# Kernel tuning notes

Hardware: AMD Instinct MI355X
Metric: run time of the kernel (lower is better)

Reference implementation:

```python
import jax, jax.numpy as jnp
import numpy as np

B = 128
N_ATOMS = 4096
NB, NA, NT = 4095, 4094, 4093
MAX_LEN = 5 * NT  # 20465, longest packed column (torsions)
EPS = 1e-8


def setup_inputs() -> dict:
    key = jax.random.key(0)
    ks = jax.random.split(key, 24)
    feats = jnp.zeros((B, MAX_LEN, 9), jnp.float32)
    # col 0: atom type ids
    atoms = jax.random.randint(ks[0], (B, N_ATOMS), 0, 6)
    # col 5: coords, flattened (N_ATOMS, 3)
    coords = jax.random.normal(ks[1], (B, N_ATOMS, 3), jnp.float32) * 5.0
    # col 6: bonds (i, j, type)
    bonds = jnp.stack([
        jax.random.randint(ks[2], (B, NB), 0, N_ATOMS),
        jax.random.randint(ks[3], (B, NB), 0, N_ATOMS),
        jax.random.randint(ks[4], (B, NB), 0, 15)], axis=-1)
    # col 7: angles (i, j, k, type)
    angles = jnp.stack([
        jax.random.randint(ks[5], (B, NA), 0, N_ATOMS),
        jax.random.randint(ks[6], (B, NA), 0, N_ATOMS),
        jax.random.randint(ks[7], (B, NA), 0, N_ATOMS),
        jax.random.randint(ks[8], (B, NA), 0, 13)], axis=-1)
    # col 8: torsions (i, j, k, l, type)
    tors = jnp.stack([
        jax.random.randint(ks[9], (B, NT), 0, N_ATOMS),
        jax.random.randint(ks[10], (B, NT), 0, N_ATOMS),
        jax.random.randint(ks[11], (B, NT), 0, N_ATOMS),
        jax.random.randint(ks[12], (B, NT), 0, N_ATOMS),
        jax.random.randint(ks[13], (B, NT), 0, 25)], axis=-1)
    feats = feats.at[:, :N_ATOMS, 0].set(atoms.astype(jnp.float32))
    feats = feats.at[:, :3 * N_ATOMS, 5].set(coords.reshape(B, -1))
    feats = feats.at[:, :3 * NB, 6].set(bonds.reshape(B, -1).astype(jnp.float32))
    feats = feats.at[:, :4 * NA, 7].set(angles.reshape(B, -1).astype(jnp.float32))
    feats = feats.at[:, :5 * NT, 8].set(tors.reshape(B, -1).astype(jnp.float32))
    lengths = jnp.tile(jnp.array(
        [[N_ATOMS, 0, 0, 0, 0, 3 * N_ATOMS, 3 * NB, 4 * NA, 5 * NT]],
        jnp.int32), (B, 1))
    bond_type = jnp.stack([jnp.ones(15), jax.random.uniform(ks[14], (15,), minval=1.0, maxval=2.0)], -1).astype(jnp.float32)
    angle_type = jnp.stack([jnp.ones(13), jax.random.uniform(ks[15], (13,), minval=1.0, maxval=3.0)], -1).astype(jnp.float32)
    tor_type = jnp.stack([jnp.ones(25), jax.random.uniform(ks[16], (25,), minval=0.0, maxval=3.14)], -1).astype(jnp.float32)
    multiplicity = jax.random.randint(ks[17], (25,), 1, 4)
    opt_pars = jax.random.uniform(ks[18], (47,), minval=0.5, maxval=1.5).astype(jnp.float32)
    return {"features": feats, "lengths": lengths, "bond_type": bond_type,
            "angle_type": angle_type, "tor_type": tor_type,
            "multiplicity": multiplicity, "opt_pars": opt_pars}


def _sample_energy(f, bond_type, angle_type, tor_type, multiplicity, opt_pars):
    coords = f[:3 * N_ATOMS, 5].reshape(-1, 3)                      # [N,3]
    bonds = f[:3 * NB, 6].astype(jnp.int32).reshape(-1, 3)          # [NB,3]
    angles = f[:4 * NA, 7].astype(jnp.int32).reshape(-1, 4)         # [NA,4]
    tors = f[:5 * NT, 8].astype(jnp.int32).reshape(-1, 5)           # [NT,5]

    # bonds: harmonic k*(r - r0)^2
    d = coords[bonds[:, 0]] - coords[bonds[:, 1]]
    r = jnp.sqrt(jnp.sum(d * d, -1) + EPS)
    pb = bond_type[bonds[:, 2]]
    e_bond = opt_pars[0] * jnp.sum(pb[:, 0] * (r - pb[:, 1]) ** 2)

    # angles: harmonic k*(theta - theta0)^2
    v1 = coords[angles[:, 0]] - coords[angles[:, 1]]
    v2 = coords[angles[:, 2]] - coords[angles[:, 1]]
    cosang = jnp.sum(v1 * v2, -1) / (
        jnp.sqrt(jnp.sum(v1 * v1, -1) + EPS) * jnp.sqrt(jnp.sum(v2 * v2, -1) + EPS))
    theta = jnp.arccos(jnp.clip(cosang, -1.0 + 1e-6, 1.0 - 1e-6))
    pa = angle_type[angles[:, 3]]
    e_ang = opt_pars[1] * jnp.sum(pa[:, 0] * (theta - pa[:, 1]) ** 2)

    # torsions: periodic k*(1 + cos(n*phi - delta))
    ci, cj, ck, cl = (coords[tors[:, m]] for m in range(4))
    b1, b2, b3 = cj - ci, ck - cj, cl - ck
    n1 = jnp.cross(b1, b2)
    n2 = jnp.cross(b2, b3)
    b2n = b2 / jnp.sqrt(jnp.sum(b2 * b2, -1, keepdims=True) + EPS)
    m1 = jnp.cross(n1, b2n)
    phi = jnp.arctan2(jnp.sum(m1 * n2, -1), jnp.sum(n1 * n2, -1))
    pt = tor_type[tors[:, 4]]
    n_mult = multiplicity[tors[:, 4]].astype(jnp.float32)
    e_tor = opt_pars[2] * jnp.sum(pt[:, 0] * (1.0 + jnp.cos(n_mult * phi - pt[:, 1])))

    return jnp.stack([e_bond, e_ang, e_tor])


def reference(features, lengths, bond_type, angle_type, tor_type, multiplicity, opt_pars):
    # lengths are uniform across batch (constants above); vmap over batch dim
    return jax.vmap(_sample_energy, in_axes=(0, None, None, None, None, None))(
        features, bond_type, angle_type, tor_type, multiplicity, opt_pars)
```

## Files before the change

kernel.cpp:

```cpp
#include <hip/hip_runtime.h>
#include <math.h>

#define BATCH   128
#define N_ATOMS 4096
#define NB      4095
#define NA      4094
#define NT      4093
#define MAX_LEN (5 * NT)
#define FSTRIDE ((size_t)MAX_LEN * 9)
#define EPSV    1e-8f
#define PARTS   6
#define THREADS 256

__global__ __launch_bounds__(THREADS) void
local_energy_kernel(const float* __restrict__ F,
                    const float* __restrict__ bond_type,
                    const float* __restrict__ angle_type,
                    const float* __restrict__ tor_type,
                    const int*   __restrict__ multiplicity,
                    const float* __restrict__ opt_pars,
                    float*       __restrict__ out)
{
    __shared__ float scx[N_ATOMS];
    __shared__ float scy[N_ATOMS];
    __shared__ float scz[N_ATOMS];
    __shared__ float sbt[30];
    __shared__ float sat[26];
    __shared__ float stt[50];
    __shared__ float smu[25];
    __shared__ float sred[12];

    const int b   = blockIdx.x;
    const int x   = b & 7;
    const int g   = b >> 3;
    const int s   = (g & 15) * 8 + x;
    const int p   = g >> 4;
    const int tid = threadIdx.x;
    const float* __restrict__ Fb = F + (size_t)s * FSTRIDE;

    if (tid < 30)                      sbt[tid]       = bond_type[tid];
    else if (tid >= 32 && tid < 58)    sat[tid - 32]  = angle_type[tid - 32];
    else if (tid >= 64 && tid < 114)   stt[tid - 64]  = tor_type[tid - 64];
    else if (tid >= 128 && tid < 153)  smu[tid - 128] = (float)multiplicity[tid - 128];

    for (int a = tid; a < N_ATOMS; a += THREADS) {
        const float* cp = Fb + 27 * a;
        float vx = cp[5];
        float vy = cp[14];
        float vz = cp[23];
        scx[a] = vx;
        scy[a] = vy;
        scz[a] = vz;
    }
    __syncthreads();

    float e_bond = 0.0f, e_ang = 0.0f, e_tor = 0.0f;

    {
        const int chunk = (NB + PARTS - 1) / PARTS;
        const int lo = p * chunk;
        const int hi = (lo + chunk < NB) ? (lo + chunk) : NB;
        for (int i = lo + tid; i < hi; i += THREADS) {
            const float* bp = Fb + 27 * i + 6;
            int a0 = (int)bp[0];
            int a1 = (int)bp[9];
            int bt = (int)bp[18];
            float dx = scx[a0] - scx[a1];
            float dy = scy[a0] - scy[a1];
            float dz = scz[a0] - scz[a1];
            float r  = sqrtf(dx*dx + dy*dy + dz*dz + EPSV);
            float k0 = sbt[bt * 2 + 0];
            float r0 = sbt[bt * 2 + 1];
            float t  = r - r0;
            e_bond += k0 * t * t;
        }
    }

    {
        const int chunk = (NA + PARTS - 1) / PARTS;
        const int lo = p * chunk;
        const int hi = (lo + chunk < NA) ? (lo + chunk) : NA;
        for (int i = lo + tid; i < hi; i += THREADS) {
            const float* ap = Fb + 36 * i + 7;
            int a0 = (int)ap[0];
            int a1 = (int)ap[9];
            int a2 = (int)ap[18];
            int at = (int)ap[27];
            float v1x = scx[a0] - scx[a1];
            float v1y = scy[a0] - scy[a1];
            float v1z = scz[a0] - scz[a1];
            float v2x = scx[a2] - scx[a1];
            float v2y = scy[a2] - scy[a1];
            float v2z = scz[a2] - scz[a1];
            float d12 = v1x*v2x + v1y*v2y + v1z*v2z;
            float n1  = sqrtf(v1x*v1x + v1y*v1y + v1z*v1z + EPSV);
            float n2  = sqrtf(v2x*v2x + v2y*v2y + v2z*v2z + EPSV);
            float cosang = d12 / (n1 * n2);
            cosang = fminf(fmaxf(cosang, -1.0f + 1e-6f), 1.0f - 1e-6f);
            float theta = acosf(cosang);
            float k0 = sat[at * 2 + 0];
            float t0 = sat[at * 2 + 1];
            float t  = theta - t0;
            e_ang += k0 * t * t;
        }
    }

    {
        const int chunk = (NT + PARTS - 1) / PARTS;
        const int lo = p * chunk;
        const int hi = (lo + chunk < NT) ? (lo + chunk) : NT;
        for (int i = lo + tid; i < hi; i += THREADS) {
            const float* tp = Fb + 45 * i + 8;
            int ai = (int)tp[0];
            int aj = (int)tp[9];
            int ak = (int)tp[18];
            int al = (int)tp[27];
            int tt = (int)tp[36];

            float cix = scx[ai], ciy = scy[ai], ciz = scz[ai];
            float cjx = scx[aj], cjy = scy[aj], cjz = scz[aj];
            float ckx = scx[ak], cky = scy[ak], ckz = scz[ak];
            float clx = scx[al], cly = scy[al], clz = scz[al];

            float b1x = cjx - cix, b1y = cjy - ciy, b1z = cjz - ciz;
            float b2x = ckx - cjx, b2y = cky - cjy, b2z = ckz - cjz;
            float b3x = clx - ckx, b3y = cly - cky, b3z = clz - ckz;

            float n1x = b1y*b2z - b1z*b2y;
            float n1y = b1z*b2x - b1x*b2z;
            float n1z = b1x*b2y - b1y*b2x;
            float n2x = b2y*b3z - b2z*b3y;
            float n2y = b2z*b3x - b2x*b3z;
            float n2z = b2x*b3y - b2y*b3x;

            float b2len = sqrtf(b2x*b2x + b2y*b2y + b2z*b2z + EPSV);
            float inv   = 1.0f / b2len;
            float bnx = b2x * inv, bny = b2y * inv, bnz = b2z * inv;

            float m1x = n1y*bnz - n1z*bny;
            float m1y = n1z*bnx - n1x*bnz;
            float m1z = n1x*bny - n1y*bnx;

            float sy = m1x*n2x + m1y*n2y + m1z*n2z;
            float sx = n1x*n2x + n1y*n2y + n1z*n2z;
            float phi = atan2f(sy, sx);

            float k0  = stt[tt * 2 + 0];
            float ph0 = stt[tt * 2 + 1];
            float nm  = smu[tt];
            e_tor += k0 * (1.0f + cosf(nm * phi - ph0));
        }
    }

    for (int off = 32; off > 0; off >>= 1) {
        e_bond += __shfl_down(e_bond, off);
        e_ang  += __shfl_down(e_ang,  off);
        e_tor  += __shfl_down(e_tor,  off);
    }
    const int wave = tid >> 6;
    const int lane = tid & 63;
    if (lane == 0) {
        sred[wave * 3 + 0] = e_bond;
        sred[wave * 3 + 1] = e_ang;
        sred[wave * 3 + 2] = e_tor;
    }
    __syncthreads();
    if (tid == 0) {
        float eb = 0.0f, ea = 0.0f, et = 0.0f;
        for (int w = 0; w < THREADS / 64; ++w) {
            eb += sred[w * 3 + 0];
            ea += sred[w * 3 + 1];
            et += sred[w * 3 + 2];
        }
        atomicAdd(&out[s * 3 + 0], opt_pars[0] * eb);
        atomicAdd(&out[s * 3 + 1], opt_pars[1] * ea);
        atomicAdd(&out[s * 3 + 2], opt_pars[2] * et);
    }
}

extern "C" void kernel_launch(void* const* d_in, const int* in_sizes, int n_in,
                              void* d_out, int out_size, void* d_ws, size_t ws_size,
                              hipStream_t stream) {
    const float* F            = (const float*)d_in[0];
    const float* bond_type    = (const float*)d_in[2];
    const float* angle_type   = (const float*)d_in[3];
    const float* tor_type     = (const float*)d_in[4];
    const int*   multiplicity = (const int*)  d_in[5];
    const float* opt_pars     = (const float*)d_in[6];
    float* out = (float*)d_out;

    hipMemsetAsync(out, 0, (size_t)out_size * sizeof(float), stream);

    dim3 grid(BATCH * PARTS);
    dim3 block(THREADS);
    local_energy_kernel<<<grid, block, 0, stream>>>(
        F, bond_type, angle_type, tor_type, multiplicity, opt_pars, out);
}
```

Before: 174.0 us.

## Stage feature rows through shared-memory tiles with coalesced float4 loads

Replaces strided scalar global reads of the interleaved 9-column feature array with cooperative, coalesced float4 copies of contiguous row tiles into LDS. Threads then pick their columns out of shared memory. The per-sample split drops from 6 to 4 parts with a fixed 1024-element chunk. This reads the full rows (all 9 columns) instead of only the needed column, adds many block barriers and extra LDS, and lowers occupancy and grid parallelism.

```diff
diff --git a/kernel.cpp b/kernel.cpp
--- a/kernel.cpp
+++ b/kernel.cpp
@@ -1,16 +1,19 @@
 #include <hip/hip_runtime.h>
 #include <math.h>
 
-#define BATCH   128
-#define N_ATOMS 4096
-#define NB      4095
-#define NA      4094
-#define NT      4093
-#define MAX_LEN (5 * NT)
-#define FSTRIDE ((size_t)MAX_LEN * 9)
-#define EPSV    1e-8f
-#define PARTS   6
-#define THREADS 256
+#define BATCH    128
+#define N_ATOMS  4096
+#define NB       4095
+#define NA       4094
+#define NT       4093
+#define MAX_LEN  (5 * NT)
+#define FSTRIDE  ((size_t)MAX_LEN * 9)
+#define TOTAL_F4 ((size_t)BATCH * FSTRIDE / 4)
+#define EPSV     1e-8f
+#define PARTS    4
+#define THREADS  256
+#define TILE_F   6916
+#define TILE_F4  1729
 
 __global__ __launch_bounds__(THREADS) void
 local_energy_kernel(const float* __restrict__ F,
@@ -24,6 +27,7 @@
     __shared__ float scx[N_ATOMS];
     __shared__ float scy[N_ATOMS];
     __shared__ float scz[N_ATOMS];
+    __shared__ __align__(16) float tile[TILE_F];
     __shared__ float sbt[30];
     __shared__ float sat[26];
     __shared__ float stt[50];
@@ -36,119 +40,155 @@
     const int s   = (g & 15) * 8 + x;
     const int p   = g >> 4;
     const int tid = threadIdx.x;
-    const float* __restrict__ Fb = F + (size_t)s * FSTRIDE;
+    const size_t sbase = (size_t)s * FSTRIDE;
 
     if (tid < 30)                      sbt[tid]       = bond_type[tid];
     else if (tid >= 32 && tid < 58)    sat[tid - 32]  = angle_type[tid - 32];
     else if (tid >= 64 && tid < 114)   stt[tid - 64]  = tor_type[tid - 64];
     else if (tid >= 128 && tid < 153)  smu[tid - 128] = (float)multiplicity[tid - 128];
 
-    for (int a = tid; a < N_ATOMS; a += THREADS) {
-        const float* cp = Fb + 27 * a;
-        float vx = cp[5];
-        float vy = cp[14];
-        float vz = cp[23];
-        scx[a] = vx;
-        scy[a] = vy;
-        scz[a] = vz;
-    }
-    __syncthreads();
+
+    for (int t = 0; t < 16; ++t) {
+        const size_t gf  = sbase + (size_t)t * 6912;
+        const size_t gf0 = gf & ~(size_t)3;
+        const int d      = (int)(gf - gf0);
+        const float4* __restrict__ src4 = (const float4*)(F + gf0);
+        const size_t q0 = gf0 >> 2;
+        for (int k = tid; k < TILE_F4; k += THREADS) {
+            if (q0 + k < TOTAL_F4) ((float4*)tile)[k] = src4[k];
+        }
+        __syncthreads();
+        const int a = 256 * t + tid;
+        scx[a] = tile[d + 27 * tid + 5];
+        scy[a] = tile[d + 27 * tid + 14];
+        scz[a] = tile[d + 27 * tid + 23];
+        __syncthreads();
+    }
 
     float e_bond = 0.0f, e_ang = 0.0f, e_tor = 0.0f;
+    const int chunk = 1024;
+    const int lo = p * chunk;
 
     {
-        const int chunk = (NB + PARTS - 1) / PARTS;
-        const int lo = p * chunk;
-        const int hi = (lo + chunk < NB) ? (lo + chunk) : NB;
-        for (int i = lo + tid; i < hi; i += THREADS) {
-            const float* bp = Fb + 27 * i + 6;
-            int a0 = (int)bp[0];
-            int a1 = (int)bp[9];
-            int bt = (int)bp[18];
-            float dx = scx[a0] - scx[a1];
-            float dy = scy[a0] - scy[a1];
-            float dz = scz[a0] - scz[a1];
-            float r  = sqrtf(dx*dx + dy*dy + dz*dz + EPSV);
-            float k0 = sbt[bt * 2 + 0];
-            float r0 = sbt[bt * 2 + 1];
-            float t  = r - r0;
-            e_bond += k0 * t * t;
+        const int hi = (lo + chunk < NB) ? lo + chunk : NB;
+        for (int it = 0; it < 4; ++it) {
+            const int e0 = lo + 256 * it;
+            if (e0 >= hi) break;
+            const size_t gf  = sbase + (size_t)27 * e0;
+            const size_t gf0 = gf & ~(size_t)3;
+            const int d      = (int)(gf - gf0);
+            const float4* __restrict__ src4 = (const float4*)(F + gf0);
+            const size_t q0 = gf0 >> 2;
+            for (int k = tid; k < TILE_F4; k += THREADS) {
+                if (q0 + k < TOTAL_F4) ((float4*)tile)[k] = src4[k];
+            }
+            __syncthreads();
+            const int e = e0 + tid;
+            if (e < hi) {
+                const int base = d + 27 * tid;
+                int a0 = (int)tile[base + 6];
+                int a1 = (int)tile[base + 15];
+                int bt = (int)tile[base + 24];
+                float dx = scx[a0] - scx[a1];
+                float dy = scy[a0] - scy[a1];
+                float dz = scz[a0] - scz[a1];
+                float r  = sqrtf(dx*dx + dy*dy + dz*dz + EPSV);
+                float t0 = r - sbt[bt * 2 + 1];
+                e_bond += sbt[bt * 2 + 0] * t0 * t0;
+            }
+            __syncthreads();
         }
     }
 
     {
-        const int chunk = (NA + PARTS - 1) / PARTS;
-        const int lo = p * chunk;
-        const int hi = (lo + chunk < NA) ? (lo + chunk) : NA;
-        for (int i = lo + tid; i < hi; i += THREADS) {
-            const float* ap = Fb + 36 * i + 7;
-            int a0 = (int)ap[0];
-            int a1 = (int)ap[9];
-            int a2 = (int)ap[18];
-            int at = (int)ap[27];
-            float v1x = scx[a0] - scx[a1];
-            float v1y = scy[a0] - scy[a1];
-            float v1z = scz[a0] - scz[a1];
-            float v2x = scx[a2] - scx[a1];
-            float v2y = scy[a2] - scy[a1];
-            float v2z = scz[a2] - scz[a1];
-            float d12 = v1x*v2x + v1y*v2y + v1z*v2z;
-            float n1  = sqrtf(v1x*v1x + v1y*v1y + v1z*v1z + EPSV);
-            float n2  = sqrtf(v2x*v2x + v2y*v2y + v2z*v2z + EPSV);
-            float cosang = d12 / (n1 * n2);
-            cosang = fminf(fmaxf(cosang, -1.0f + 1e-6f), 1.0f - 1e-6f);
-            float theta = acosf(cosang);
-            float k0 = sat[at * 2 + 0];
-            float t0 = sat[at * 2 + 1];
-            float t  = theta - t0;
-            e_ang += k0 * t * t;
+        const int hi = (lo + chunk < NA) ? lo + chunk : NA;
+        for (int it = 0; it < 6; ++it) {
+            const int e0 = lo + 192 * it;
+            if (e0 >= hi) break;
+            const size_t gf  = sbase + (size_t)36 * e0;
+            const size_t gf0 = gf & ~(size_t)3;
+            const int d      = (int)(gf - gf0);
+            const float4* __restrict__ src4 = (const float4*)(F + gf0);
+            const size_t q0 = gf0 >> 2;
+            for (int k = tid; k < TILE_F4; k += THREADS) {
+                if (q0 + k < TOTAL_F4) ((float4*)tile)[k] = src4[k];
+            }
+            __syncthreads();
+            const int e = e0 + tid;
+            if (tid < 192 && e < hi) {
+                const int base = d + 36 * tid;
+                int a0 = (int)tile[base + 7];
+                int a1 = (int)tile[base + 16];
+                int a2 = (int)tile[base + 25];
+                int at = (int)tile[base + 34];
+                float v1x = scx[a0] - scx[a1];
+                float v1y = scy[a0] - scy[a1];
+                float v1z = scz[a0] - scz[a1];
+                float v2x = scx[a2] - scx[a1];
+                float v2y = scy[a2] - scy[a1];
+                float v2z = scz[a2] - scz[a1];
+                float d12 = v1x*v2x + v1y*v2y + v1z*v2z;
+                float n1  = sqrtf(v1x*v1x + v1y*v1y + v1z*v1z + EPSV);
+                float n2  = sqrtf(v2x*v2x + v2y*v2y + v2z*v2z + EPSV);
+                float cosang = d12 / (n1 * n2);
+                cosang = fminf(fmaxf(cosang, -1.0f + 1e-6f), 1.0f - 1e-6f);
+                float theta = acosf(cosang);
+                float t0 = theta - sat[at * 2 + 1];
+                e_ang += sat[at * 2 + 0] * t0 * t0;
+            }
+            __syncthreads();
         }
     }
 
     {
-        const int chunk = (NT + PARTS - 1) / PARTS;
-        const int lo = p * chunk;
-        const int hi = (lo + chunk < NT) ? (lo + chunk) : NT;
-        for (int i = lo + tid; i < hi; i += THREADS) {
-            const float* tp = Fb + 45 * i + 8;
-            int ai = (int)tp[0];
-            int aj = (int)tp[9];
-            int ak = (int)tp[18];
-            int al = (int)tp[27];
-            int tt = (int)tp[36];
-
-            float cix = scx[ai], ciy = scy[ai], ciz = scz[ai];
-            float cjx = scx[aj], cjy = scy[aj], cjz = scz[aj];
-            float ckx = scx[ak], cky = scy[ak], ckz = scz[ak];
-            float clx = scx[al], cly = scy[al], clz = scz[al];
-
-            float b1x = cjx - cix, b1y = cjy - ciy, b1z = cjz - ciz;
-            float b2x = ckx - cjx, b2y = cky - cjy, b2z = ckz - cjz;
-            float b3x = clx - ckx, b3y = cly - cky, b3z = clz - ckz;
-
-            float n1x = b1y*b2z - b1z*b2y;
-            float n1y = b1z*b2x - b1x*b2z;
-            float n1z = b1x*b2y - b1y*b2x;
-            float n2x = b2y*b3z - b2z*b3y;
-            float n2y = b2z*b3x - b2x*b3z;
-            float n2z = b2x*b3y - b2y*b3x;
-
-            float b2len = sqrtf(b2x*b2x + b2y*b2y + b2z*b2z + EPSV);
-            float inv   = 1.0f / b2len;
-            float bnx = b2x * inv, bny = b2y * inv, bnz = b2z * inv;
-
-            float m1x = n1y*bnz - n1z*bny;
-            float m1y = n1z*bnx - n1x*bnz;
-            float m1z = n1x*bny - n1y*bnx;
-
-            float sy = m1x*n2x + m1y*n2y + m1z*n2z;
-            float sx = n1x*n2x + n1y*n2y + n1z*n2z;
-            float phi = atan2f(sy, sx);
-
-            float k0  = stt[tt * 2 + 0];
-            float ph0 = stt[tt * 2 + 1];
-            float nm  = smu[tt];
-            e_tor += k0 * (1.0f + cosf(nm * phi - ph0));
+        const int hi = (lo + chunk < NT) ? lo + chunk : NT;
+        for (int it = 0; it < 8; ++it) {
+            const int e0 = lo + 144 * it;
+            if (e0 >= hi) break;
+            const size_t gf  = sbase + (size_t)45 * e0;
+            const size_t gf0 = gf & ~(size_t)3;
+            const int d      = (int)(gf - gf0);
+            const float4* __restrict__ src4 = (const float4*)(F + gf0);
+            const size_t q0 = gf0 >> 2;
+            const int nf4 = (45 * 144 + d + 3) >> 2;
+            for (int k = tid; k < nf4; k += THREADS) {
+                if (q0 + k < TOTAL_F4) ((float4*)tile)[k] = src4[k];
+            }
+            __syncthreads();
+            const int e = e0 + tid;
+            if (tid < 144 && e < hi) {
+                const int base = d + 45 * tid;
+                int ai = (int)tile[base + 8];
+                int aj = (int)tile[base + 17];
+                int ak = (int)tile[base + 26];
+                int al = (int)tile[base + 35];
+                int tt = (int)tile[base + 44];
+
+                float b1x = scx[aj] - scx[ai], b1y = scy[aj] - scy[ai], b1z = scz[aj] - scz[ai];
+                float b2x = scx[ak] - scx[aj], b2y = scy[ak] - scy[aj], b2z = scz[ak] - scz[aj];
+                float b3x = scx[al] - scx[ak], b3y = scy[al] - scy[ak], b3z = scz[al] - scz[ak];
+
+                float n1x = b1y*b2z - b1z*b2y;
+                float n1y = b1z*b2x - b1x*b2z;
+                float n1z = b1x*b2y - b1y*b2x;
+                float n2x = b2y*b3z - b2z*b3y;
+                float n2y = b2z*b3x - b2x*b3z;
+                float n2z = b2x*b3y - b2y*b3x;
+
+                float inv = 1.0f / sqrtf(b2x*b2x + b2y*b2y + b2z*b2z + EPSV);
+                float bnx = b2x * inv, bny = b2y * inv, bnz = b2z * inv;
+
+                float m1x = n1y*bnz - n1z*bny;
+                float m1y = n1z*bnx - n1x*bnz;
+                float m1z = n1x*bny - n1y*bnx;
+
+                float sy = m1x*n2x + m1y*n2y + m1z*n2z;
+                float sx = n1x*n2x + n1y*n2y + n1z*n2z;
+                float phi = atan2f(sy, sx);
+
+                e_tor += stt[tt * 2 + 0] * (1.0f + cosf(smu[tt] * phi - stt[tt * 2 + 1]));
+            }
+            __syncthreads();
         }
     }
 
```

Measured after the change: 258.1 us. 48.3% more time.

## Stream feature rows in float4 tiles through per-wave LDS with register prefetch

Applied to the files above, without the earlier changes.

Replaces strided scalar global loads with coalesced float4 tile loads of whole feature rows (1080 floats, covering 40 atoms/bonds, 30 angles, 24 torsions) that each wave stages in its own LDS slice. Bond, angle and torsion terms are then computed from the same staged tile, so each row is read from global memory once instead of three times with strided access. The next tile is prefetched into registers. The grid shrinks to 2 blocks of 1024 threads per sample. This trades occupancy and lane utilisation (only 24-40 of 64 lanes compute per tile) for far fewer global memory transactions.

```diff
diff --git a/kernel.cpp b/kernel.cpp
--- a/kernel.cpp
+++ b/kernel.cpp
@@ -1,34 +1,40 @@
 #include <hip/hip_runtime.h>
 #include <math.h>
 
-#define BATCH   128
-#define N_ATOMS 4096
-#define NB      4095
-#define NA      4094
-#define NT      4093
-#define MAX_LEN (5 * NT)
-#define FSTRIDE ((size_t)MAX_LEN * 9)
-#define EPSV    1e-8f
-#define PARTS   6
-#define THREADS 256
-
-__global__ __launch_bounds__(THREADS) void
-local_energy_kernel(const float* __restrict__ F,
-                    const float* __restrict__ bond_type,
-                    const float* __restrict__ angle_type,
-                    const float* __restrict__ tor_type,
-                    const int*   __restrict__ multiplicity,
-                    const float* __restrict__ opt_pars,
-                    float*       __restrict__ out)
+#define BATCH      128
+#define N_ATOMS    4096
+#define NB         4095
+#define NA         4094
+#define NT         4093
+#define FSTRIDE    184185
+#define COORD_SPAN 110592
+#define TOTAL_F4   5893920u
+#define EPSV       1e-8f
+#define THREADS    1024
+#define WAVES      16
+#define TILE_F     1080
+#define NTILES     171
+#define CTILES     103
+#define SCR_F4     272
+
+#define WAVE_LDS_FENCE()  do { asm volatile("" ::: "memory"); \
+                               __builtin_amdgcn_wave_barrier(); } while (0)
+
+__global__ __launch_bounds__(THREADS, 1) void
+local_energy_fused(const float* __restrict__ F,
+                   const float* __restrict__ bond_type,
+                   const float* __restrict__ angle_type,
+                   const float* __restrict__ tor_type,
+                   const int*   __restrict__ multiplicity,
+                   const float* __restrict__ opt_pars,
+                   float*       __restrict__ out)
 {
     __shared__ float scx[N_ATOMS];
     __shared__ float scy[N_ATOMS];
     __shared__ float scz[N_ATOMS];
-    __shared__ float sbt[30];
-    __shared__ float sat[26];
-    __shared__ float stt[50];
-    __shared__ float smu[25];
-    __shared__ float sred[12];
+    __shared__ __align__(16) float4 scr[WAVES][SCR_F4];
+    __shared__ float sbt[30], sat[26], stt[50], smu[25];
+    __shared__ float sred[WAVES * 3];
 
     const int b   = blockIdx.x;
     const int x   = b & 7;
@@ -36,119 +42,178 @@
     const int s   = (g & 15) * 8 + x;
     const int p   = g >> 4;
     const int tid = threadIdx.x;
-    const float* __restrict__ Fb = F + (size_t)s * FSTRIDE;
+    const int w   = tid >> 6;
+    const int l   = tid & 63;
+    const size_t sbase = (size_t)s * FSTRIDE;
+    const int d = (int)(sbase & 3);
+    const float4* __restrict__ F4 = (const float4*)F;
 
     if (tid < 30)                      sbt[tid]       = bond_type[tid];
     else if (tid >= 32 && tid < 58)    sat[tid - 32]  = angle_type[tid - 32];
     else if (tid >= 64 && tid < 114)   stt[tid - 64]  = tor_type[tid - 64];
     else if (tid >= 128 && tid < 153)  smu[tid - 128] = (float)multiplicity[tid - 128];
 
-    for (int a = tid; a < N_ATOMS; a += THREADS) {
-        const float* cp = Fb + 27 * a;
-        float vx = cp[5];
-        float vy = cp[14];
-        float vz = cp[23];
-        scx[a] = vx;
-        scy[a] = vy;
-        scz[a] = vz;
+    float* const swf = (float*)scr[w];
+
+    {
+        float4 cur[5];
+        int t = w;
+        {
+            const size_t q0 = (sbase + (size_t)t * TILE_F) >> 2;
+            const int nf = (COORD_SPAN - t * TILE_F < TILE_F) ? COORD_SPAN - t * TILE_F : TILE_F;
+            const int nq = (d + nf + 3) >> 2;
+            #pragma unroll
+            for (int i = 0; i < 5; ++i) {
+                const int k = l + 64 * i;
+                cur[i] = (k < nq && q0 + k < TOTAL_F4) ? F4[q0 + k]
+                                                       : make_float4(0.f, 0.f, 0.f, 0.f);
+            }
+        }
+        for (; t < CTILES; t += WAVES) {
+            const int tn = t + WAVES;
+            float4 nxt[5];
+            #pragma unroll
+            for (int i = 0; i < 5; ++i) nxt[i] = make_float4(0.f, 0.f, 0.f, 0.f);
+            if (tn < CTILES) {
+                const size_t q0 = (sbase + (size_t)tn * TILE_F) >> 2;
+                const int nf = (COORD_SPAN - tn * TILE_F < TILE_F) ? COORD_SPAN - tn * TILE_F : TILE_F;
+                const int nq = (d + nf + 3) >> 2;
+                #pragma unroll
+                for (int i = 0; i < 5; ++i) {
+                    const int k = l + 64 * i;
+                    if (k < nq && q0 + k < TOTAL_F4) nxt[i] = F4[q0 + k];
+                }
+            }
+            #pragma unroll
+            for (int i = 0; i < 4; ++i) scr[w][l + 64 * i] = cur[i];
+            if (l < 15) scr[w][l + 256] = cur[4];
+            WAVE_LDS_FENCE();
+
+            const int na = (N_ATOMS - 40 * t < 40) ? N_ATOMS - 40 * t : 40;
+            if (l < na) {
+                const int base = d + 27 * l;
+                const int atom = 40 * t + l;
+                scx[atom] = swf[base + 5];
+                scy[atom] = swf[base + 14];
+                scz[atom] = swf[base + 23];
+            }
+            WAVE_LDS_FENCE();
+            #pragma unroll
+            for (int i = 0; i < 5; ++i) cur[i] = nxt[i];
+        }
     }
     __syncthreads();
 
-    float e_bond = 0.0f, e_ang = 0.0f, e_tor = 0.0f;
-
+    float e_bond = 0.f, e_ang = 0.f, e_tor = 0.f;
     {
-        const int chunk = (NB + PARTS - 1) / PARTS;
-        const int lo = p * chunk;
-        const int hi = (lo + chunk < NB) ? (lo + chunk) : NB;
-        for (int i = lo + tid; i < hi; i += THREADS) {
-            const float* bp = Fb + 27 * i + 6;
-            int a0 = (int)bp[0];
-            int a1 = (int)bp[9];
-            int bt = (int)bp[18];
-            float dx = scx[a0] - scx[a1];
-            float dy = scy[a0] - scy[a1];
-            float dz = scz[a0] - scz[a1];
-            float r  = sqrtf(dx*dx + dy*dy + dz*dz + EPSV);
-            float k0 = sbt[bt * 2 + 0];
-            float r0 = sbt[bt * 2 + 1];
-            float t  = r - r0;
-            e_bond += k0 * t * t;
-        }
-    }
-
-    {
-        const int chunk = (NA + PARTS - 1) / PARTS;
-        const int lo = p * chunk;
-        const int hi = (lo + chunk < NA) ? (lo + chunk) : NA;
-        for (int i = lo + tid; i < hi; i += THREADS) {
-            const float* ap = Fb + 36 * i + 7;
-            int a0 = (int)ap[0];
-            int a1 = (int)ap[9];
-            int a2 = (int)ap[18];
-            int at = (int)ap[27];
-            float v1x = scx[a0] - scx[a1];
-            float v1y = scy[a0] - scy[a1];
-            float v1z = scz[a0] - scz[a1];
-            float v2x = scx[a2] - scx[a1];
-            float v2y = scy[a2] - scy[a1];
-            float v2z = scz[a2] - scz[a1];
-            float d12 = v1x*v2x + v1y*v2y + v1z*v2z;
-            float n1  = sqrtf(v1x*v1x + v1y*v1y + v1z*v1z + EPSV);
-            float n2  = sqrtf(v2x*v2x + v2y*v2y + v2z*v2z + EPSV);
-            float cosang = d12 / (n1 * n2);
-            cosang = fminf(fmaxf(cosang, -1.0f + 1e-6f), 1.0f - 1e-6f);
-            float theta = acosf(cosang);
-            float k0 = sat[at * 2 + 0];
-            float t0 = sat[at * 2 + 1];
-            float t  = theta - t0;
-            e_ang += k0 * t * t;
-        }
-    }
-
-    {
-        const int chunk = (NT + PARTS - 1) / PARTS;
-        const int lo = p * chunk;
-        const int hi = (lo + chunk < NT) ? (lo + chunk) : NT;
-        for (int i = lo + tid; i < hi; i += THREADS) {
-            const float* tp = Fb + 45 * i + 8;
-            int ai = (int)tp[0];
-            int aj = (int)tp[9];
-            int ak = (int)tp[18];
-            int al = (int)tp[27];
-            int tt = (int)tp[36];
-
-            float cix = scx[ai], ciy = scy[ai], ciz = scz[ai];
-            float cjx = scx[aj], cjy = scy[aj], cjz = scz[aj];
-            float ckx = scx[ak], cky = scy[ak], ckz = scz[ak];
-            float clx = scx[al], cly = scy[al], clz = scz[al];
-
-            float b1x = cjx - cix, b1y = cjy - ciy, b1z = cjz - ciz;
-            float b2x = ckx - cjx, b2y = cky - cjy, b2z = ckz - cjz;
-            float b3x = clx - ckx, b3y = cly - cky, b3z = clz - ckz;
-
-            float n1x = b1y*b2z - b1z*b2y;
-            float n1y = b1z*b2x - b1x*b2z;
-            float n1z = b1x*b2y - b1y*b2x;
-            float n2x = b2y*b3z - b2z*b3y;
-            float n2y = b2z*b3x - b2x*b3z;
-            float n2z = b2x*b3y - b2y*b3x;
-
-            float b2len = sqrtf(b2x*b2x + b2y*b2y + b2z*b2z + EPSV);
-            float inv   = 1.0f / b2len;
-            float bnx = b2x * inv, bny = b2y * inv, bnz = b2z * inv;
-
-            float m1x = n1y*bnz - n1z*bny;
-            float m1y = n1z*bnx - n1x*bnz;
-            float m1z = n1x*bny - n1y*bnx;
-
-            float sy = m1x*n2x + m1y*n2y + m1z*n2z;
-            float sx = n1x*n2x + n1y*n2y + n1z*n2z;
-            float phi = atan2f(sy, sx);
-
-            float k0  = stt[tt * 2 + 0];
-            float ph0 = stt[tt * 2 + 1];
-            float nm  = smu[tt];
-            e_tor += k0 * (1.0f + cosf(nm * phi - ph0));
+        const int tlo = (p == 0) ? 0  : 86;
+        const int thi = (p == 0) ? 86 : NTILES;
+        float4 cur[5];
+        int t = tlo + w;
+        if (t < thi) {
+            const size_t q0 = (sbase + (size_t)t * TILE_F) >> 2;
+            const int nf = (FSTRIDE - t * TILE_F < TILE_F) ? FSTRIDE - t * TILE_F : TILE_F;
+            const int nq = (d + nf + 3) >> 2;
+            #pragma unroll
+            for (int i = 0; i < 5; ++i) {
+                const int k = l + 64 * i;
+                cur[i] = (k < nq && q0 + k < TOTAL_F4) ? F4[q0 + k]
+                                                       : make_float4(0.f, 0.f, 0.f, 0.f);
+            }
+        }
+        for (; t < thi; t += WAVES) {
+            const int tn = t + WAVES;
+            float4 nxt[5];
+            #pragma unroll
+            for (int i = 0; i < 5; ++i) nxt[i] = make_float4(0.f, 0.f, 0.f, 0.f);
+            if (tn < thi) {
+                const size_t q0 = (sbase + (size_t)tn * TILE_F) >> 2;
+                const int nf = (FSTRIDE - tn * TILE_F < TILE_F) ? FSTRIDE - tn * TILE_F : TILE_F;
+                const int nq = (d + nf + 3) >> 2;
+                #pragma unroll
+                for (int i = 0; i < 5; ++i) {
+                    const int k = l + 64 * i;
+                    if (k < nq && q0 + k < TOTAL_F4) nxt[i] = F4[q0 + k];
+                }
+            }
+            #pragma unroll
+            for (int i = 0; i < 4; ++i) scr[w][l + 64 * i] = cur[i];
+            if (l < 15) scr[w][l + 256] = cur[4];
+            WAVE_LDS_FENCE();
+
+            int nb = NB - 40 * t; nb = (nb > 40) ? 40 : nb;
+            if (l < nb) {
+                const int base = d + 27 * l;
+                const int a0 = (int)swf[base + 6];
+                const int a1 = (int)swf[base + 15];
+                const int bt = (int)swf[base + 24];
+                const float dx = scx[a0] - scx[a1];
+                const float dy = scy[a0] - scy[a1];
+                const float dz = scz[a0] - scz[a1];
+                const float r  = sqrtf(dx*dx + dy*dy + dz*dz + EPSV);
+                const float t0 = r - sbt[bt * 2 + 1];
+                e_bond += sbt[bt * 2 + 0] * t0 * t0;
+            }
+
+            int na = NA - 30 * t; na = (na > 30) ? 30 : na;
+            if (l < na) {
+                const int base = d + 36 * l;
+                const int a0 = (int)swf[base + 7];
+                const int a1 = (int)swf[base + 16];
+                const int a2 = (int)swf[base + 25];
+                const int at = (int)swf[base + 34];
+                const float v1x = scx[a0] - scx[a1];
+                const float v1y = scy[a0] - scy[a1];
+                const float v1z = scz[a0] - scz[a1];
+                const float v2x = scx[a2] - scx[a1];
+                const float v2y = scy[a2] - scy[a1];
+                const float v2z = scz[a2] - scz[a1];
+                const float d12 = v1x*v2x + v1y*v2y + v1z*v2z;
+                const float n1  = sqrtf(v1x*v1x + v1y*v1y + v1z*v1z + EPSV);
+                const float n2  = sqrtf(v2x*v2x + v2y*v2y + v2z*v2z + EPSV);
+                float cosang = d12 / (n1 * n2);
+                cosang = fminf(fmaxf(cosang, -1.0f + 1e-6f), 1.0f - 1e-6f);
+                const float t0 = acosf(cosang) - sat[at * 2 + 1];
+                e_ang += sat[at * 2 + 0] * t0 * t0;
+            }
+
+            int ntr = NT - 24 * t; ntr = (ntr > 24) ? 24 : ntr;
+            if (l < ntr) {
+                const int base = d + 45 * l;
+                const int ai = (int)swf[base + 8];
+                const int aj = (int)swf[base + 17];
+                const int ak = (int)swf[base + 26];
+                const int al = (int)swf[base + 35];
+                const int tt = (int)swf[base + 44];
+
+                const float b1x = scx[aj] - scx[ai], b1y = scy[aj] - scy[ai], b1z = scz[aj] - scz[ai];
+                const float b2x = scx[ak] - scx[aj], b2y = scy[ak] - scy[aj], b2z = scz[ak] - scz[aj];
+                const float b3x = scx[al] - scx[ak], b3y = scy[al] - scy[ak], b3z = scz[al] - scz[ak];
+
+                const float n1x = b1y*b2z - b1z*b2y;
+                const float n1y = b1z*b2x - b1x*b2z;
+                const float n1z = b1x*b2y - b1y*b2x;
+                const float n2x = b2y*b3z - b2z*b3y;
+                const float n2y = b2z*b3x - b2x*b3z;
+                const float n2z = b2x*b3y - b2y*b3x;
+
+                const float inv = 1.0f / sqrtf(b2x*b2x + b2y*b2y + b2z*b2z + EPSV);
+                const float bnx = b2x * inv, bny = b2y * inv, bnz = b2z * inv;
+
+                const float m1x = n1y*bnz - n1z*bny;
+                const float m1y = n1z*bnx - n1x*bnz;
+                const float m1z = n1x*bny - n1y*bnx;
+
+                const float sy = m1x*n2x + m1y*n2y + m1z*n2z;
+                const float sx = n1x*n2x + n1y*n2y + n1z*n2z;
+                const float phi = atan2f(sy, sx);
+
+                e_tor += stt[tt * 2 + 0] * (1.0f + cosf(smu[tt] * phi - stt[tt * 2 + 1]));
+            }
+
+            WAVE_LDS_FENCE();
+            #pragma unroll
+            for (int i = 0; i < 5; ++i) cur[i] = nxt[i];
         }
     }
 
@@ -157,20 +222,18 @@
         e_ang  += __shfl_down(e_ang,  off);
         e_tor  += __shfl_down(e_tor,  off);
     }
-    const int wave = tid >> 6;
-    const int lane = tid & 63;
-    if (lane == 0) {
-        sred[wave * 3 + 0] = e_bond;
-        sred[wave * 3 + 1] = e_ang;
-        sred[wave * 3 + 2] = e_tor;
+    if (l == 0) {
+        sred[w * 3 + 0] = e_bond;
+        sred[w * 3 + 1] = e_ang;
+        sred[w * 3 + 2] = e_tor;
     }
     __syncthreads();
     if (tid == 0) {
-        float eb = 0.0f, ea = 0.0f, et = 0.0f;
-        for (int w = 0; w < THREADS / 64; ++w) {
-            eb += sred[w * 3 + 0];
-            ea += sred[w * 3 + 1];
-            et += sred[w * 3 + 2];
+        float eb = 0.f, ea = 0.f, et = 0.f;
+        for (int i = 0; i < WAVES; ++i) {
+            eb += sred[i * 3 + 0];
+            ea += sred[i * 3 + 1];
+            et += sred[i * 3 + 2];
         }
         atomicAdd(&out[s * 3 + 0], opt_pars[0] * eb);
         atomicAdd(&out[s * 3 + 1], opt_pars[1] * ea);
@@ -191,8 +254,6 @@
 
     hipMemsetAsync(out, 0, (size_t)out_size * sizeof(float), stream);
 
-    dim3 grid(BATCH * PARTS);
-    dim3 block(THREADS);
-    local_energy_kernel<<<grid, block, 0, stream>>>(
+    local_energy_fused<<<dim3(BATCH * 2), dim3(THREADS), 0, stream>>>(
         F, bond_type, angle_type, tor_type, multiplicity, opt_pars, out);
 }
```

New measurement: 158.3 us. -9.0%, faster.
